# Kernel tuning notes

Measured on AMD Instinct MI355X. Metric: run time of the kernel, lower is better.

## Reference

```python
import jax, jax.numpy as jnp
import numpy as np

B, S, D, H = 2, 2048, 1024, 16
DK = D // H
LN_EPS = 1e-5


def setup_inputs() -> dict:
    key = jax.random.key(0)
    ks = jax.random.split(key, 10)
    scale = 1.0 / np.sqrt(D)
    return {
        "input_Q": jax.random.normal(ks[0], (B, S, D), jnp.float32),
        "input_K": jax.random.normal(ks[1], (B, S, D), jnp.float32),
        "input_V": jax.random.normal(ks[2], (B, S, D), jnp.float32),
        "mask": jax.random.randint(ks[3], (B, S, S), 0, 2, jnp.int32),
        "W_Q": jax.random.normal(ks[4], (D, D), jnp.float32) * scale,
        "W_K": jax.random.normal(ks[5], (D, D), jnp.float32) * scale,
        "W_V": jax.random.normal(ks[6], (D, D), jnp.float32) * scale,
        "W_O": jax.random.normal(ks[7], (D, D), jnp.float32) * scale,
        "ln_gamma": jnp.ones((D,), jnp.float32),
        "ln_beta": jnp.zeros((D,), jnp.float32),
    }


def reference(input_Q, input_K, input_V, mask, W_Q, W_K, W_V, W_O, ln_gamma, ln_beta):
    # projections -> [B, H, S, DK]
    q = (input_Q @ W_Q).reshape(B, S, H, DK).transpose(0, 2, 1, 3)
    k = (input_K @ W_K).reshape(B, S, H, DK).transpose(0, 2, 1, 3)
    v = (input_V @ W_V).reshape(B, S, H, DK).transpose(0, 2, 1, 3)

    # explicit O(S^2) scores as in the original module
    scores = jnp.einsum("bhqd,bhkd->bhqk", q, k) / np.sqrt(DK)
    scores = jnp.where(mask[:, None, :, :].astype(bool), -1e9, scores)
    attn = jax.nn.softmax(scores, axis=-1)
    ctx = jnp.einsum("bhqk,bhkd->bhqd", attn, v)

    # merge heads, output projection, residual + LayerNorm
    ctx = ctx.transpose(0, 2, 1, 3).reshape(B, S, D)
    out = ctx @ W_O + input_Q
    mu = out.mean(-1, keepdims=True)
    var = jnp.mean((out - mu) ** 2, -1, keepdims=True)
    return (out - mu) * jax.lax.rsqrt(var + LN_EPS) * ln_gamma + ln_beta
```

## Files before the change

kernel.cpp:

```cpp
#include <hip/hip_runtime.h>

typedef __bf16 bf16x8 __attribute__((ext_vector_type(8)));
typedef float  f32x4  __attribute__((ext_vector_type(4)));
typedef short  s16x2  __attribute__((ext_vector_type(2)));

#define AS1 __attribute__((address_space(1)))
#define AS3 __attribute__((address_space(3)))

__device__ __forceinline__ void g2l16(const void* g, void* l) {
  __builtin_amdgcn_global_load_lds((AS1 void*)g, (AS3 void*)l, 16, 0, 0);
}
#define MFMA16(a, b, c) __builtin_amdgcn_mfma_f32_16x16x32_bf16(a, b, c, 0, 0, 0)

__device__ __forceinline__ unsigned pack_bf16(float a, float b) {
  union { __bf16 h[2]; unsigned u; } p;
  p.h[0] = (__bf16)a; p.h[1] = (__bf16)b;
  return p.u;
}

__global__ __launch_bounds__(256) void prep(const float* __restrict__ inQ,
    const float* __restrict__ inK, const float* __restrict__ inV,
    const int* __restrict__ mask,
    const float* __restrict__ W0, const float* __restrict__ W1,
    const float* __restrict__ W2, const float* __restrict__ W3,
    __bf16* __restrict__ Xq, __bf16* __restrict__ Xk, __bf16* __restrict__ Xv,
    unsigned long long* __restrict__ bits, __bf16* __restrict__ Wt) {
  __shared__ __bf16 tile[64][65];
  const int blk = blockIdx.x;
  if (blk < 6144) {
    const int z = blk >> 11, bx = blk & 2047;
    const float* src = z == 0 ? inQ : (z == 1 ? inK : inV);
    __bf16* dst = z == 0 ? Xq : (z == 1 ? Xk : Xv);
    size_t base = ((size_t)bx * 256 + threadIdx.x) * 8;
    float4 f0 = *(const float4*)(src + base);
    float4 f1 = *(const float4*)(src + base + 4);
    bf16x8 o;
    o[0] = (__bf16)f0.x; o[1] = (__bf16)f0.y; o[2] = (__bf16)f0.z; o[3] = (__bf16)f0.w;
    o[4] = (__bf16)f1.x; o[5] = (__bf16)f1.y; o[6] = (__bf16)f1.z; o[7] = (__bf16)f1.w;
    *(bf16x8*)(dst + base) = o;
  } else if (blk < 10240) {
    const int lane = threadIdx.x & 63, w = threadIdx.x >> 6;
    const int base = (blk - 6144) * 2048 + w * 512;
#pragma unroll
    for (int it = 0; it < 8; ++it) {
      int i = base + it * 64 + lane;
      unsigned long long bb = __ballot(mask[i] == 0);
      if (lane == 0) bits[i >> 6] = bb;
    }
  } else {
    const int idx = blk - 10240;
    const int z = idx >> 8, rem = idx & 255, bx = rem & 15, by = rem >> 4;
    const float* srcs[4] = {W0, W1, W2, W3};
    const float* src = srcs[z];
    __bf16* dst = Wt + (size_t)z * 1024 * 1024;
    int cb = bx * 64, rb = by * 64;
    for (int i = threadIdx.x; i < 4096; i += 256) {
      int r = i >> 6, c = i & 63;
      tile[r][c] = (__bf16)src[(size_t)(rb + r) * 1024 + cb + c];
    }
    __syncthreads();
    for (int i = threadIdx.x; i < 4096; i += 256) {
      int c = i >> 6, r = i & 63;
      dst[(size_t)(cb + c) * 1024 + rb + r] = tile[r][c];
    }
  }
}

__global__ __launch_bounds__(256) void qkv_gemm(const __bf16* __restrict__ Xq,
    const __bf16* __restrict__ Xk, const __bf16* __restrict__ Xv,
    const __bf16* __restrict__ Wt, __bf16* __restrict__ Qb,
    __bf16* __restrict__ Kb, __bf16* __restrict__ Vtb) {
  __shared__ __align__(16) __bf16 sh[8192];
  __bf16* As = sh;
  __bf16* Bs = sh + 4096;
  const int z = blockIdx.z;
  const __bf16* X = z == 0 ? Xq : (z == 1 ? Xk : Xv);
  const __bf16* W = Wt + (size_t)z * 1048576;
  const float scale = z == 0 ? 0.125f * 1.44269504088896f : 1.f;
  const int t = threadIdx.x;
  const int lane = t & 63, w = t >> 6;
  const int lane15 = lane & 15, quad = lane >> 4;
  const int wm = (w >> 1) * 64, wn = (w & 1) * 64;
  const int mBase = blockIdx.y * 128, nBase = blockIdx.x * 128;
  const int c1 = t, c2 = t + 256;
  f32x4 acc[4][4] = {};
  for (int kt = 0; kt < 1024; kt += 32) {
    __syncthreads();
    g2l16(X + (size_t)(mBase + (c1 >> 2)) * 1024 + kt + (c1 & 3) * 8, As + c1 * 8);
    g2l16(X + (size_t)(mBase + (c2 >> 2)) * 1024 + kt + (c2 & 3) * 8, As + c2 * 8);
    g2l16(W + (size_t)(nBase + (c1 >> 2)) * 1024 + kt + (c1 & 3) * 8, Bs + c1 * 8);
    g2l16(W + (size_t)(nBase + (c2 >> 2)) * 1024 + kt + (c2 & 3) * 8, Bs + c2 * 8);
    __builtin_amdgcn_s_waitcnt(0);
    __syncthreads();
    bf16x8 a[4], b[4];
#pragma unroll
    for (int i = 0; i < 4; i++) a[i] = *(const bf16x8*)&As[(wm + i * 16 + lane15) * 32 + quad * 8];
#pragma unroll
    for (int j = 0; j < 4; j++) b[j] = *(const bf16x8*)&Bs[(wn + j * 16 + lane15) * 32 + quad * 8];
#pragma unroll
    for (int i = 0; i < 4; i++)
#pragma unroll
      for (int j = 0; j < 4; j++)
        acc[i][j] = MFMA16(a[i], b[j], acc[i][j]);
  }
  if (z != 2) {
    __bf16* Y = z == 0 ? Qb : Kb;
#pragma unroll
    for (int i = 0; i < 4; i++)
#pragma unroll
      for (int j = 0; j < 4; j++)
#pragma unroll
        for (int r = 0; r < 4; r++) {
          int mg = mBase + wm + i * 16 + quad * 4 + r;
          int ng = nBase + wn + j * 16 + lane15;
          int b_ = mg >> 11, s_ = mg & 2047, h_ = ng >> 6, d_ = ng & 63;
          Y[(((size_t)(b_ * 16 + h_)) * 2048 + s_) * 64 + d_] = (__bf16)(acc[i][j][r] * scale);
        }
  } else {
    const int s0 = mBase & 2047;
    const int bhBase = (mBase >> 11) * 16 + (nBase >> 6);
#pragma unroll
    for (int half = 0; half < 2; ++half) {
      __syncthreads();
      if ((w & 1) == half) {
#pragma unroll
        for (int i = 0; i < 4; i++)
#pragma unroll
          for (int j = 0; j < 4; j++)
#pragma unroll
            for (int r = 0; r < 4; r++) {
              int nl = j * 16 + lane15;
              int ml = wm + i * 16 + quad * 4 + r;
              int l5 = ml & 31;
              int mlp = (ml & 96) | ((((l5 >> 2) & 3) * 8) + ((l5 & 3) * 2) + ((l5 >> 4) & 1));
              sh[nl * 128 + (mlp ^ ((nl & 7) * 16))] = (__bf16)acc[i][j][r];
            }
      }
      __syncthreads();
      const int row = t >> 2, c0 = (t & 3) * 32;
      const int xr = (row & 7) * 16;
      const int b0 = row * 128 + (c0 ^ xr);
      const int b1 = row * 128 + ((c0 + 16) ^ xr);
      bf16x8 a0 = *(const bf16x8*)&sh[b0];
      bf16x8 a1 = *(const bf16x8*)&sh[b0 + 8];
      bf16x8 a2 = *(const bf16x8*)&sh[b1];
      bf16x8 a3 = *(const bf16x8*)&sh[b1 + 8];
      __bf16* dst = Vtb + (size_t)(bhBase + half) * 131072 + (size_t)row * 2048 + s0 + c0;
      *(bf16x8*)(dst)      = a0;
      *(bf16x8*)(dst + 8)  = a1;
      *(bf16x8*)(dst + 16) = a2;
      *(bf16x8*)(dst + 24) = a3;
    }
  }
}

__global__ __launch_bounds__(256) void gemm_wo(const __bf16* __restrict__ X,
    const __bf16* __restrict__ Wt, const float* __restrict__ resid,
    float* __restrict__ Yf) {
  __shared__ __align__(16) __bf16 As[64 * 32];
  __shared__ __align__(16) __bf16 Bs[128 * 32];
  const int t = threadIdx.x;
  const int lane = t & 63, w = t >> 6;
  const int lane15 = lane & 15, quad = lane >> 4;
  const int wm = (w >> 1) * 32, wn = (w & 1) * 64;
  const int mBase = blockIdx.y * 64, nBase = blockIdx.x * 128;
  f32x4 acc[2][4] = {};
  for (int kt = 0; kt < 1024; kt += 32) {
    __syncthreads();
    g2l16(X  + (size_t)(mBase + (t >> 2)) * 1024 + kt + (t & 3) * 8, As + t * 8);
    g2l16(Wt + (size_t)(nBase + (t >> 2)) * 1024 + kt + (t & 3) * 8, Bs + t * 8);
    g2l16(Wt + (size_t)(nBase + ((t + 256) >> 2)) * 1024 + kt + (t & 3) * 8, Bs + (t + 256) * 8);
    __builtin_amdgcn_s_waitcnt(0);
    __syncthreads();
    bf16x8 a[2], b[4];
#pragma unroll
    for (int i = 0; i < 2; i++) a[i] = *(const bf16x8*)&As[(wm + i * 16 + lane15) * 32 + quad * 8];
#pragma unroll
    for (int j = 0; j < 4; j++) b[j] = *(const bf16x8*)&Bs[(wn + j * 16 + lane15) * 32 + quad * 8];
#pragma unroll
    for (int i = 0; i < 2; i++)
#pragma unroll
      for (int j = 0; j < 4; j++)
        acc[i][j] = MFMA16(a[i], b[j], acc[i][j]);
  }
#pragma unroll
  for (int i = 0; i < 2; i++)
#pragma unroll
    for (int j = 0; j < 4; j++)
#pragma unroll
      for (int r = 0; r < 4; r++) {
        int mg = mBase + wm + i * 16 + quad * 4 + r;
        int ng = nBase + wn + j * 16 + lane15;
        size_t idx = (size_t)mg * 1024 + ng;
        Yf[idx] = acc[i][j][r] + resid[idx];
      }
}

__global__ __launch_bounds__(256, 4) void attn_kernel(const __bf16* __restrict__ Q,
    const __bf16* __restrict__ Kp, const __bf16* __restrict__ Vt,
    const unsigned* __restrict__ mbits, __bf16* __restrict__ ctx) {
  __shared__ __align__(16) __bf16 Qs[64 * 64];
  __shared__ __align__(16) __bf16 Ks[4][32 * 64];
  __shared__ __align__(16) __bf16 Vs[4][64 * 32];
  const int t = threadIdx.x, lane = t & 63, w = t >> 6;
  const int l15 = lane & 15, quad = lane >> 4;
  const int bh = blockIdx.y, b = bh >> 4, h = bh & 15;
  const int qBase = blockIdx.x * 64;
  const size_t qko = (size_t)bh * 2048 * 64;
  const size_t vko = (size_t)bh * 64 * 2048;
  const int srow8 = lane >> 3, sch8 = (lane & 7) ^ srow8;
  const int srow16 = lane >> 2, sch4 = (lane & 3) ^ ((lane >> 3) & 3);
  const int stOff = w * 512 + lane * 8;
  const __bf16* kSrc = Kp + qko + (size_t)(w * 8 + srow8) * 64 + sch8 * 8;
  const __bf16* vSrc = Vt + vko + (size_t)(w * 16 + srow16) * 2048 + sch4 * 8;
  __bf16* KsF = &Ks[0][0];
  __bf16* VsF = &Vs[0][0];
  g2l16(Q + qko + (size_t)(qBase + w * 8 + srow8) * 64 + sch8 * 8,       Qs + w * 512 + lane * 8);
  g2l16(Q + qko + (size_t)(qBase + (w + 4) * 8 + srow8) * 64 + sch8 * 8, Qs + (w + 4) * 512 + lane * 8);
  g2l16(kSrc,        KsF + stOff);
  g2l16(vSrc,        VsF + stOff);
  g2l16(kSrc + 2048, KsF + 2048 + stOff);
  g2l16(vSrc + 32,   VsF + 2048 + stOff);
  const size_t mIdx = ((size_t)b * 2048 + qBase + w * 16 + l15) * 64;
  unsigned m32 = mbits[mIdx];
  __builtin_amdgcn_s_waitcnt(0);
  __syncthreads();
  bf16x8 qb0, qb1;
  {
    const int r = w * 16 + l15, s = r & 7;
    qb0 = *(const bf16x8*)&Qs[r * 64 + ((quad ^ s) * 8)];
    qb1 = *(const bf16x8*)&Qs[r * 64 + (((4 + quad) ^ s) * 8)];
  }
  const int sA = l15 & 7, trB = 16 + l15, sB = trB & 7;
  const int offA0 = l15 * 64 + ((quad ^ sA) * 8);
  const int offA1 = l15 * 64 + (((4 + quad) ^ sA) * 8);
  const int offB0 = trB * 64 + ((quad ^ sB) * 8);
  const int offB1 = trB * 64 + (((4 + quad) ^ sB) * 8);
  bf16x8 kr0[2][2], kr1[2][2];
  kr0[0][0] = *(const bf16x8*)&KsF[offA0];
  kr0[0][1] = *(const bf16x8*)&KsF[offA1];
  kr0[1][0] = *(const bf16x8*)&KsF[offB0];
  kr0[1][1] = *(const bf16x8*)&KsF[offB1];
  bf16x8 ones;
#pragma unroll
  for (int i = 0; i < 8; i++) ones[i] = (__bf16)1.0f;
  f32x4 o[4] = {};
  f32x4 ol = {};
  bf16x8 pa;

#define ATTN_BODY(KT, KCUR, KNXT)                                                   \
  {                                                                                 \
    __syncthreads();    \
    if ((KT) < 62) {                                                                \
      const int sl = ((KT) + 2) & 3;                                                \
      g2l16(kSrc + (size_t)((KT) + 2) * 2048, KsF + sl * 2048 + stOff);             \
      g2l16(vSrc + ((KT) + 2) * 32,           VsF + sl * 2048 + stOff);             \
    }                                                                               \
    unsigned mnext = 0;                                                             \
    if ((KT) < 63) mnext = mbits[mIdx + (KT) + 1];                                  \
       \
    f32x4 st0, st1;                                                                 \
    {                                                                               \
      f32x4 zz = {0.f, 0.f, 0.f, 0.f};                                              \
      zz  = MFMA16(KCUR[0][0], qb0, zz);                                            \
      st0 = MFMA16(KCUR[0][1], qb1, zz);                                            \
      f32x4 zy = {0.f, 0.f, 0.f, 0.f};                                              \
      zy  = MFMA16(KCUR[1][0], qb0, zy);                                            \
      st1 = MFMA16(KCUR[1][1], qb1, zy);                                            \
    }                                                                               \
             \
    if ((KT) > 0) {                                                                 \
      const __bf16* Vb = VsF + (((KT) - 1) & 3) * 2048;                             \
      ol = MFMA16(pa, ones, ol);                                                    \
      _Pragma("unroll")                                                             \
      for (int j = 0; j < 4; j++) {                                                 \
        const int dr = j * 16 + l15;                                                \
        bf16x8 vb = *(const bf16x8*)&Vb[dr * 32 + ((quad ^ ((dr >> 1) & 3)) * 8)];  \
        o[j] = MFMA16(pa, vb, o[j]);                                                \
      }                                                                             \
    }                                                                               \
               \
    if ((KT) < 63) {                                                                \
      const __bf16* Kn = KsF + (((KT) + 1) & 3) * 2048;                             \
      KNXT[0][0] = *(const bf16x8*)&Kn[offA0];                                      \
      KNXT[0][1] = *(const bf16x8*)&Kn[offA1];                                      \
      KNXT[1][0] = *(const bf16x8*)&Kn[offB0];                                      \
      KNXT[1][1] = *(const bf16x8*)&Kn[offB1];                                      \
    }                                                                               \
       \
    {                                                                               \
      const unsigned msh = m32 >> (quad * 4);                                       \
      union { unsigned u[4]; bf16x8 v; } pk;                                        \
      _Pragma("unroll")                                                             \
      for (int r = 0; r < 4; r++) {                                                 \
        float e0 = __builtin_exp2f(st0[r]);                                         \
        float e1 = __builtin_exp2f(st1[r]);                                         \
        union { unsigned u; s16x2 s; } mc;                                          \
        mc.u = msh << (15 - r);                                                     \
        mc.s = mc.s >> 15;                                 \
        pk.u[r] = pack_bf16(e0, e1) & mc.u;                                         \
      }                                                                             \
      pa = pk.v;                                                                    \
    }                                                                               \
    m32 = mnext;                                                                    \
  }

  for (int kt = 0; kt < 64; kt += 2) {
    ATTN_BODY(kt,     kr0, kr1);
    ATTN_BODY(kt + 1, kr1, kr0);
  }
#undef ATTN_BODY

  {
    const __bf16* Vb = VsF + (63 & 3) * 2048;
    ol = MFMA16(pa, ones, ol);
#pragma unroll
    for (int j = 0; j < 4; j++) {
      const int dr = j * 16 + l15;
      bf16x8 vb = *(const bf16x8*)&Vb[dr * 32 + ((quad ^ ((dr >> 1) & 3)) * 8)];
      o[j] = MFMA16(pa, vb, o[j]);
    }
  }
#pragma unroll
  for (int r = 0; r < 4; r++) {
    float inv = 1.f / ol[r];
    int qg = qBase + w * 16 + quad * 4 + r;
    size_t base = ((size_t)b * 2048 + qg) * 1024 + h * 64;
#pragma unroll
    for (int j = 0; j < 4; j++)
      ctx[base + j * 16 + l15] = (__bf16)(o[j][r] * inv);
  }
}

__global__ __launch_bounds__(256) void ln_kernel(const float* __restrict__ X,
    const float* __restrict__ gamma, const float* __restrict__ beta,
    float* __restrict__ out) {
  __shared__ float red[8];
  const int t = threadIdx.x;
  const size_t row = blockIdx.x;
  const float* xr = X + row * 1024;
  float4 x = *(const float4*)(xr + t * 4);
  float s = x.x + x.y + x.z + x.w;
  float s2 = x.x * x.x + x.y * x.y + x.z * x.z + x.w * x.w;
#pragma unroll
  for (int off = 1; off < 64; off <<= 1) { s += __shfl_xor(s, off); s2 += __shfl_xor(s2, off); }
  if ((t & 63) == 0) { red[t >> 6] = s; red[4 + (t >> 6)] = s2; }
  __syncthreads();
  float S1 = red[0] + red[1] + red[2] + red[3];
  float S2 = red[4] + red[5] + red[6] + red[7];
  float mu = S1 * (1.f / 1024.f);
  float var = S2 * (1.f / 1024.f) - mu * mu;
  float rs = rsqrtf(var + 1e-5f);
  float4 g = *(const float4*)(gamma + t * 4);
  float4 bb = *(const float4*)(beta + t * 4);
  float4 y;
  y.x = (x.x - mu) * rs * g.x + bb.x;
  y.y = (x.y - mu) * rs * g.y + bb.y;
  y.z = (x.z - mu) * rs * g.z + bb.z;
  y.w = (x.w - mu) * rs * g.w + bb.w;
  *(float4*)(out + row * 1024 + t * 4) = y;
}

extern "C" void kernel_launch(void* const* d_in, const int* in_sizes, int n_in,
                              void* d_out, int out_size, void* d_ws, size_t ws_size,
                              hipStream_t stream) {
  const float* inQ  = (const float*)d_in[0];
  const float* inK  = (const float*)d_in[1];
  const float* inV  = (const float*)d_in[2];
  const int*   mask = (const int*)d_in[3];
  const float* WQ   = (const float*)d_in[4];
  const float* WK   = (const float*)d_in[5];
  const float* WV   = (const float*)d_in[6];
  const float* WO   = (const float*)d_in[7];
  const float* gamma = (const float*)d_in[8];
  const float* beta  = (const float*)d_in[9];

  const size_t MB = 1024 * 1024;
  char* ws = (char*)d_ws;
  __bf16* Xq  = (__bf16*)(ws);
  __bf16* Xk  = (__bf16*)(ws + 8 * MB);
  __bf16* Xv  = (__bf16*)(ws + 16 * MB);
  __bf16* Qb  = (__bf16*)(ws + 24 * MB);
  __bf16* Kb  = (__bf16*)(ws + 32 * MB);
  __bf16* Vtb = (__bf16*)(ws + 48 * MB);
  __bf16* Wt  = (__bf16*)(ws + 56 * MB);
  unsigned long long* mbits = (unsigned long long*)(ws + 64 * MB);
  __bf16* ctx  = Xq;
  float*  outp = (float*)(ws + 8 * MB);

  prep<<<dim3(11264), 256, 0, stream>>>(inQ, inK, inV, mask, WQ, WK, WV, WO,
                                        Xq, Xk, Xv, mbits, Wt);
  qkv_gemm<<<dim3(8, 32, 3), 256, 0, stream>>>(Xq, Xk, Xv, Wt, Qb, Kb, Vtb);
  attn_kernel<<<dim3(32, 32), 256, 0, stream>>>(Qb, Kb, Vtb, (const unsigned*)mbits, ctx);
  gemm_wo<<<dim3(8, 64), 256, 0, stream>>>(ctx, Wt + 3 * 1048576, inQ, outp);
  ln_kernel<<<dim3(4096), 256, 0, stream>>>(outp, gamma, beta, (float*)d_out);
}
```

Baseline: 288.2 us.

## Deepen attention software pipeline and remap blocks for head-grouped scheduling

The attention loop becomes a three-stage software pipeline. QK^T for tile kt runs alongside the exp/mask of tile kt-1 and the PV MFMAs of tile kt-2, with V fragments preloaded into registers a step ahead. This is meant to hide exp and LDS-read latency behind MFMA work. Block indices are also remapped so consecutive blocks spread across heads, which may change L2 reuse of K/V. The cost is more live registers (extra score, probability and V buffers), which could hurt occupancy under the launch bound of 4.

```diff
diff --git a/kernel.cpp b/kernel.cpp
--- a/kernel.cpp
+++ b/kernel.cpp
@@ -204,8 +204,11 @@
   __shared__ __align__(16) __bf16 Vs[4][64 * 32];
   const int t = threadIdx.x, lane = t & 63, w = t >> 6;
   const int l15 = lane & 15, quad = lane >> 4;
-  const int bh = blockIdx.y, b = bh >> 4, h = bh & 15;
-  const int qBase = blockIdx.x * 64;
+  const int id = blockIdx.x + (blockIdx.y << 5);
+  const int iix = id >> 3;
+  const int bh = (id & 7) * 4 + (iix >> 5);
+  const int qBase = (iix & 31) * 64;
+  const int b = bh >> 4, h = bh & 15;
   const size_t qko = (size_t)bh * 2048 * 64;
   const size_t vko = (size_t)bh * 64 * 2048;
   const int srow8 = lane >> 3, sch8 = (lane & 7) ^ srow8;
@@ -221,8 +224,11 @@
   g2l16(vSrc,        VsF + stOff);
   g2l16(kSrc + 2048, KsF + 2048 + stOff);
   g2l16(vSrc + 32,   VsF + 2048 + stOff);
+  const __bf16* kStage = kSrc + 2 * 2048;
+  const __bf16* vStage = vSrc + 2 * 32;
   const size_t mIdx = ((size_t)b * 2048 + qBase + w * 16 + l15) * 64;
-  unsigned m32 = mbits[mIdx];
+  unsigned mCur = mbits[mIdx];
+  unsigned mPrev = 0;
   __builtin_amdgcn_s_waitcnt(0);
   __syncthreads();
   bf16x8 qb0, qb1;
@@ -236,90 +242,119 @@
   const int offA1 = l15 * 64 + (((4 + quad) ^ sA) * 8);
   const int offB0 = trB * 64 + ((quad ^ sB) * 8);
   const int offB1 = trB * 64 + (((4 + quad) ^ sB) * 8);
-  bf16x8 kr0[2][2], kr1[2][2];
-  kr0[0][0] = *(const bf16x8*)&KsF[offA0];
-  kr0[0][1] = *(const bf16x8*)&KsF[offA1];
-  kr0[1][0] = *(const bf16x8*)&KsF[offB0];
-  kr0[1][1] = *(const bf16x8*)&KsF[offB1];
+  const int dr0 = l15,      voff0 = dr0 * 32 + ((quad ^ ((dr0 >> 1) & 3)) * 8);
+  const int dr1 = 16 + l15, voff1 = dr1 * 32 + ((quad ^ ((dr1 >> 1) & 3)) * 8);
+  const int dr2 = 32 + l15, voff2 = dr2 * 32 + ((quad ^ ((dr2 >> 1) & 3)) * 8);
+  const int dr3 = 48 + l15, voff3 = dr3 * 32 + ((quad ^ ((dr3 >> 1) & 3)) * 8);
+  bf16x8 krA[2][2], krB[2][2];
+  krA[0][0] = *(const bf16x8*)&KsF[offA0];
+  krA[0][1] = *(const bf16x8*)&KsF[offA1];
+  krA[1][0] = *(const bf16x8*)&KsF[offB0];
+  krA[1][1] = *(const bf16x8*)&KsF[offB1];
   bf16x8 ones;
 #pragma unroll
   for (int i = 0; i < 8; i++) ones[i] = (__bf16)1.0f;
   f32x4 o[4] = {};
   f32x4 ol = {};
-  bf16x8 pa;
-
-#define ATTN_BODY(KT, KCUR, KNXT)                                                   \
+  f32x4 stA[2] = {}, stB[2] = {};
+  bf16x8 paA = {}, paB = {};
+  bf16x8 vrA[4] = {}, vrB[4] = {};
+
+#define ATTN_BODY(KT, KC, KN, STO, STI, PAO, PAI, VRO, VRI)                         \
   {                                                                                 \
-    __syncthreads();    \
+    __syncthreads();                 \
     if ((KT) < 62) {                                                                \
       const int sl = ((KT) + 2) & 3;                                                \
-      g2l16(kSrc + (size_t)((KT) + 2) * 2048, KsF + sl * 2048 + stOff);             \
-      g2l16(vSrc + ((KT) + 2) * 32,           VsF + sl * 2048 + stOff);             \
-    }                                                                               \
-    unsigned mnext = 0;                                                             \
-    if ((KT) < 63) mnext = mbits[mIdx + (KT) + 1];                                  \
-       \
-    f32x4 st0, st1;                                                                 \
+      g2l16(kStage, KsF + sl * 2048 + stOff); kStage += 2048;                       \
+      g2l16(vStage, VsF + sl * 2048 + stOff); vStage += 32;                         \
+    }                                                                               \
+    unsigned mNew = 0;                                                              \
+    if ((KT) < 63) mNew = mbits[mIdx + (KT) + 1];                                   \
+                \
     {                                                                               \
       f32x4 zz = {0.f, 0.f, 0.f, 0.f};                                              \
-      zz  = MFMA16(KCUR[0][0], qb0, zz);                                            \
-      st0 = MFMA16(KCUR[0][1], qb1, zz);                                            \
+      zz     = MFMA16(KC[0][0], qb0, zz);                                           \
+      STO[0] = MFMA16(KC[0][1], qb1, zz);                                           \
       f32x4 zy = {0.f, 0.f, 0.f, 0.f};                                              \
-      zy  = MFMA16(KCUR[1][0], qb0, zy);                                            \
-      st1 = MFMA16(KCUR[1][1], qb1, zy);                                            \
-    }                                                                               \
-             \
-    if ((KT) > 0) {                                                                 \
-      const __bf16* Vb = VsF + (((KT) - 1) & 3) * 2048;                             \
-      ol = MFMA16(pa, ones, ol);                                                    \
-      _Pragma("unroll")                                                             \
-      for (int j = 0; j < 4; j++) {                                                 \
-        const int dr = j * 16 + l15;                                                \
-        bf16x8 vb = *(const bf16x8*)&Vb[dr * 32 + ((quad ^ ((dr >> 1) & 3)) * 8)];  \
-        o[j] = MFMA16(pa, vb, o[j]);                                                \
-      }                                                                             \
-    }                                                                               \
-               \
+      zy     = MFMA16(KC[1][0], qb0, zy);                                           \
+      STO[1] = MFMA16(KC[1][1], qb1, zy);                                           \
+    }                                                                               \
+                                  \
+    if ((KT) >= 2) {                                                                \
+      ol   = MFMA16(PAI, ones,   ol);                                               \
+      o[0] = MFMA16(PAI, VRI[0], o[0]);                                             \
+      o[1] = MFMA16(PAI, VRI[1], o[1]);                                             \
+      o[2] = MFMA16(PAI, VRI[2], o[2]);                                             \
+      o[3] = MFMA16(PAI, VRI[3], o[3]);                                             \
+    }                                                                               \
+                                                           \
     if ((KT) < 63) {                                                                \
       const __bf16* Kn = KsF + (((KT) + 1) & 3) * 2048;                             \
-      KNXT[0][0] = *(const bf16x8*)&Kn[offA0];                                      \
-      KNXT[0][1] = *(const bf16x8*)&Kn[offA1];                                      \
-      KNXT[1][0] = *(const bf16x8*)&Kn[offB0];                                      \
-      KNXT[1][1] = *(const bf16x8*)&Kn[offB1];                                      \
-    }                                                                               \
-       \
-    {                                                                               \
-      const unsigned msh = m32 >> (quad * 4);                                       \
+      KN[0][0] = *(const bf16x8*)&Kn[offA0];                                        \
+      KN[0][1] = *(const bf16x8*)&Kn[offA1];                                        \
+      KN[1][0] = *(const bf16x8*)&Kn[offB0];                                        \
+      KN[1][1] = *(const bf16x8*)&Kn[offB1];                                        \
+    }                                                                               \
+                                                           \
+    if ((KT) >= 1) {                                                                \
+      const __bf16* Vb = VsF + (((KT) - 1) & 3) * 2048;                             \
+      VRO[0] = *(const bf16x8*)&Vb[voff0];                                          \
+      VRO[1] = *(const bf16x8*)&Vb[voff1];                                          \
+      VRO[2] = *(const bf16x8*)&Vb[voff2];                                          \
+      VRO[3] = *(const bf16x8*)&Vb[voff3];                                          \
+    }                                                                               \
+                 \
+    if ((KT) >= 1) {                                                                \
+      const unsigned msh = mPrev >> (quad * 4);                                     \
       union { unsigned u[4]; bf16x8 v; } pk;                                        \
       _Pragma("unroll")                                                             \
       for (int r = 0; r < 4; r++) {                                                 \
-        float e0 = __builtin_exp2f(st0[r]);                                         \
-        float e1 = __builtin_exp2f(st1[r]);                                         \
+        float e0 = __builtin_exp2f(STI[0][r]);                                      \
+        float e1 = __builtin_exp2f(STI[1][r]);                                      \
         union { unsigned u; s16x2 s; } mc;                                          \
         mc.u = msh << (15 - r);                                                     \
-        mc.s = mc.s >> 15;                                 \
+        mc.s = mc.s >> 15;                                                          \
         pk.u[r] = pack_bf16(e0, e1) & mc.u;                                         \
       }                                                                             \
-      pa = pk.v;                                                                    \
-    }                                                                               \
-    m32 = mnext;                                                                    \
+      PAO = pk.v;                                                                   \
+    }                                                                               \
+    mPrev = mCur; mCur = mNew;                                                      \
   }
 
   for (int kt = 0; kt < 64; kt += 2) {
-    ATTN_BODY(kt,     kr0, kr1);
-    ATTN_BODY(kt + 1, kr1, kr0);
+    ATTN_BODY(kt,     krA, krB, stA, stB, paB, paA, vrB, vrA);
+    ATTN_BODY(kt + 1, krB, krA, stB, stA, paA, paB, vrA, vrB);
   }
 #undef ATTN_BODY
 
   {
-    const __bf16* Vb = VsF + (63 & 3) * 2048;
-    ol = MFMA16(pa, ones, ol);
-#pragma unroll
-    for (int j = 0; j < 4; j++) {
-      const int dr = j * 16 + l15;
-      bf16x8 vb = *(const bf16x8*)&Vb[dr * 32 + ((quad ^ ((dr >> 1) & 3)) * 8)];
-      o[j] = MFMA16(pa, vb, o[j]);
+    const __bf16* Vb = VsF + 3 * 2048;
+    vrB[0] = *(const bf16x8*)&Vb[voff0];
+    vrB[1] = *(const bf16x8*)&Vb[voff1];
+    vrB[2] = *(const bf16x8*)&Vb[voff2];
+    vrB[3] = *(const bf16x8*)&Vb[voff3];
+    ol   = MFMA16(paA, ones,   ol);
+    o[0] = MFMA16(paA, vrA[0], o[0]);
+    o[1] = MFMA16(paA, vrA[1], o[1]);
+    o[2] = MFMA16(paA, vrA[2], o[2]);
+    o[3] = MFMA16(paA, vrA[3], o[3]);
+    const unsigned msh = mPrev >> (quad * 4);
+    union { unsigned u[4]; bf16x8 v; } pk;
+#pragma unroll
+    for (int r = 0; r < 4; r++) {
+      float e0 = __builtin_exp2f(stB[0][r]);
+      float e1 = __builtin_exp2f(stB[1][r]);
+      union { unsigned u; s16x2 s; } mc;
+      mc.u = msh << (15 - r);
+      mc.s = mc.s >> 15;
+      pk.u[r] = pack_bf16(e0, e1) & mc.u;
     }
+    paB = pk.v;
+    ol   = MFMA16(paB, ones,   ol);
+    o[0] = MFMA16(paB, vrB[0], o[0]);
+    o[1] = MFMA16(paB, vrB[1], o[1]);
+    o[2] = MFMA16(paB, vrB[2], o[2]);
+    o[3] = MFMA16(paB, vrB[3], o[3]);
   }
 #pragma unroll
   for (int r = 0; r < 4; r++) {
```

Result: no change. 287.0 us (-0.4%).
